# Kernel optimization log

Measured on AMD Instinct MI355X. Metric: run time of the kernel, lower is better.

The kernel has to match this reference:

```python
import jax, jax.numpy as jnp
import numpy as np

N_NODES = 100000
N_EDGES = 1600000
IN_CH, EDGE_DIM, HIDDEN, OUT_CH = 3, 3, 64, 1


def setup_inputs() -> dict:
    key = jax.random.key(0)
    ks = jax.random.split(key, 10)
    x = jax.random.normal(ks[0], (N_NODES, IN_CH), dtype=jnp.float32)
    edge_index = jax.random.randint(ks[1], (2, N_EDGES), 0, N_NODES, dtype=jnp.int64)
    edge_attr = jax.random.normal(ks[2], (N_EDGES, EDGE_DIM), dtype=jnp.float32)
    # Linear params (torch Linear: y = x @ W.T + b); we store W as (in, out)
    s1 = 1.0 / np.sqrt(IN_CH + EDGE_DIM)
    W1 = jax.random.uniform(ks[3], (IN_CH + EDGE_DIM, HIDDEN), jnp.float32, -s1, s1)
    b1 = jax.random.uniform(ks[4], (HIDDEN,), jnp.float32, -s1, s1)
    s2 = 1.0 / np.sqrt(HIDDEN + EDGE_DIM)
    W2 = jax.random.uniform(ks[5], (HIDDEN + EDGE_DIM, HIDDEN), jnp.float32, -s2, s2)
    b2 = jax.random.uniform(ks[6], (HIDDEN,), jnp.float32, -s2, s2)
    s3 = 1.0 / np.sqrt(HIDDEN)
    W3 = jax.random.uniform(ks[7], (HIDDEN, OUT_CH), jnp.float32, -s3, s3)
    b3 = jax.random.uniform(ks[8], (OUT_CH,), jnp.float32, -s3, s3)
    return {"x": x, "edge_index": edge_index, "edge_attr": edge_attr,
            "W1": W1, "b1": b1, "W2": W2, "b2": b2, "W3": W3, "b3": b3}


def _edge_conv(h, src, dst, edge_attr, W, b, n_nodes):
    # gather source node features, concat edge_attr, linear, scatter-add at dst
    msg = jnp.concatenate([h[src], edge_attr], axis=-1) @ W + b  # [E, out]
    return jax.ops.segment_sum(msg, dst, num_segments=n_nodes)   # [N, out]


def reference(x, edge_index, edge_attr, W1, b1, W2, b2, W3, b3):
    src, dst = edge_index[0], edge_index[1]  # PyG source_to_target: aggregate at edge_index[1]
    n = x.shape[0]
    h = jax.nn.relu(_edge_conv(x, src, dst, edge_attr, W1, b1, n))
    h = jax.nn.relu(_edge_conv(h, src, dst, edge_attr, W2, b2, n))
    return h @ W3 + b3  # (n_nodes, 1) anomaly logits
```

## Files before the change

kernel.cpp:

```cpp
#include <hip/hip_runtime.h>

#define N_NODES 100000
#define N_EDGES 1600000
#define NCHUNK 256
#define CHUNK_E (N_EDGES / NCHUNK)
#define BSHIFT 6
#define BMASK 63
#define NBUCK 1563
#define REC_CAP 1536


typedef unsigned int uint4_ev __attribute__((ext_vector_type(4)));
typedef short bf16x8 __attribute__((ext_vector_type(8)));
typedef float f32x4 __attribute__((ext_vector_type(4)));

__device__ __forceinline__ unsigned short f2bf(float f) {
    unsigned int u = __float_as_uint(f);
    unsigned int r = (u + 0x7fff + ((u >> 16) & 1)) >> 16;
    return (unsigned short)r;
}
__device__ __forceinline__ unsigned int pack2bf(float a, float b) {
    return (unsigned int)f2bf(a) | ((unsigned int)f2bf(b) << 16);
}
__device__ __forceinline__ float bflo(unsigned int v) { return __uint_as_float(v << 16); }
__device__ __forceinline__ float bfhi(unsigned int v) { return __uint_as_float(v & 0xffff0000u); }

__device__ __forceinline__ float4 nt_load4(const float4* p) {
    uint4_ev v = __builtin_nontemporal_load((const uint4_ev*)p);
    return make_float4(__uint_as_float(v.x), __uint_as_float(v.y),
                       __uint_as_float(v.z), __uint_as_float(v.w));
}

__device__ __forceinline__ int wave_incl_scan(int v, int lane) {
#pragma unroll
    for (int off = 1; off < 64; off <<= 1) {
        int t = __shfl_up(v, off, 64);
        if (lane >= off) v += t;
    }
    return v;
}

__global__ __launch_bounds__(1024) void k_hist(const int* __restrict__ ei,
                                               int* __restrict__ tbl,
                                               const float* __restrict__ W2,
                                               unsigned short* __restrict__ wpk) {
    if (blockIdx.x == NCHUNK) {
        int i = threadIdx.x;
        if (i < 512) {
            int lane = i & 63, hh = (i >> 6) & 1, nt = i >> 7;
            int col = nt * 16 + (lane & 15);
            int k0 = hh * 32 + (lane >> 4) * 8;
#pragma unroll
            for (int j = 0; j < 8; j++)
                wpk[i * 8 + j] = f2bf(W2[(k0 + j) * 64 + col]);
        }
        return;
    }
    __shared__ int h[NBUCK];
    for (int i = threadIdx.x; i < NBUCK; i += 1024) h[i] = 0;
    __syncthreads();
    const int base = blockIdx.x * CHUNK_E;
    for (int i = threadIdx.x; i < CHUNK_E; i += 1024)
        atomicAdd(&h[ei[N_EDGES + base + i] >> BSHIFT], 1);
    __syncthreads();
    for (int i = threadIdx.x; i < NBUCK; i += 1024)
        tbl[blockIdx.x * NBUCK + i] = h[i];
}

__global__ __launch_bounds__(256) void k_colscan(int* __restrict__ tbl,
                                                 int* __restrict__ bsum) {
    const int b = blockIdx.x, t = threadIdx.x;
    int v = tbl[t * NBUCK + b];
    int lane = t & 63, w = t >> 6;
    int inc = wave_incl_scan(v, lane);
    __shared__ int ws[4];
    if (lane == 63) ws[w] = inc;
    __syncthreads();
    int wo = 0;
    for (int k = 0; k < w; k++) wo += ws[k];
    tbl[t * NBUCK + b] = wo + inc - v;
    if (t == 255) bsum[b] = wo + inc;
}

__global__ __launch_bounds__(1024) void k_basescan(const int* __restrict__ bsum,
                                                   int* __restrict__ bbase) {
    int t = threadIdx.x, lane = t & 63, w = t >> 6;
    int i0 = 2 * t, i1 = 2 * t + 1;
    int v0 = (i0 < NBUCK) ? bsum[i0] : 0;
    int v1 = (i1 < NBUCK) ? bsum[i1] : 0;
    int s = v0 + v1;
    int inc = wave_incl_scan(s, lane);
    __shared__ int ws[16];
    if (lane == 63) ws[w] = inc;
    __syncthreads();
    int wo = 0;
    for (int k = 0; k < w; k++) wo += ws[k];
    int excl = wo + inc - s;
    if (i0 < NBUCK) bbase[i0] = excl;
    if (i1 < NBUCK) bbase[i1] = excl + v0;
    if (i0 == NBUCK - 1) bbase[NBUCK] = excl + v0;
}

__global__ __launch_bounds__(1024) void k_scatter(const int* __restrict__ ei,
                                                  const float* __restrict__ ea,
                                                  const int* __restrict__ tbl,
                                                  const int* __restrict__ bbase,
                                                  float4* __restrict__ stg) {
    __shared__ int cur[NBUCK];
    for (int i = threadIdx.x; i < NBUCK; i += 1024)
        cur[i] = tbl[blockIdx.x * NBUCK + i] + bbase[i];
    __syncthreads();
    const int base = blockIdx.x * CHUNK_E;
    for (int i = threadIdx.x; i < CHUNK_E; i += 1024) {
        int e = base + i;
        int src = ei[e];
        int dst = ei[N_EDGES + e];
        float a0 = ea[(size_t)e * 3 + 0];
        float a1 = ea[(size_t)e * 3 + 1];
        float a2 = ea[(size_t)e * 3 + 2];
        int p = atomicAdd(&cur[dst >> BSHIFT], 1);
        unsigned pk = (unsigned)src | ((unsigned)(dst & BMASK) << 17);
        stg[p] = make_float4(__uint_as_float(pk), a0, a1, a2);
    }
}

__global__ __launch_bounds__(256) void k_finalize(
    const float4* __restrict__ stg, const int* __restrict__ bbase,
    const float* __restrict__ x, int* __restrict__ csr,
    int* __restrict__ degp, int* __restrict__ rowend,
    float* __restrict__ U, float* __restrict__ T) {
    __shared__ float4 rec[REC_CAP];
    __shared__ int hist[64], lofs[64], cur[64];
    const int b = blockIdx.x, t = threadIdx.x;
    const int base = bbase[b], cnt = bbase[b + 1] - base;
    if (t < 64) hist[t] = 0;
    __syncthreads();
    const float* stgf = (const float*)stg;
    for (int i = t; i < cnt; i += 256) {
        unsigned pk = __float_as_uint(stgf[(size_t)(base + i) * 4]);
        atomicAdd(&hist[pk >> 17], 1);
    }
    __syncthreads();
    if (t < 64) {
        int v = hist[t];
        int inc = wave_incl_scan(v, t);
        lofs[t] = inc - v;
        cur[t] = inc - v;
    }
    __syncthreads();
    for (int i = t; i < cnt; i += 256) {
        float4 r = nt_load4(&stg[base + i]);
        unsigned pk = __float_as_uint(r.x);
        int p = atomicAdd(&cur[pk >> 17], 1);
        if (p < REC_CAP) rec[p] = r;
    }
    __syncthreads();
    const int l = t >> 2, sub = t & 3;
    const int n = b * 64 + l;
    const int d = hist[l], lo = lofs[l];
    float u0 = 0, u1 = 0, u2 = 0, t0 = 0, t1 = 0, t2 = 0;
    for (int j = sub; j < d; j += 4) {
        float4 r = rec[lo + j];
        unsigned pk = __float_as_uint(r.x);
        int src = pk & 0x1FFFF;
        csr[base + lo + j] = src;
        t0 += r.y; t1 += r.z; t2 += r.w;
        u0 += x[src * 3 + 0]; u1 += x[src * 3 + 1]; u2 += x[src * 3 + 2];
    }
#pragma unroll
    for (int off = 1; off <= 2; off <<= 1) {
        u0 += __shfl_xor(u0, off, 64); u1 += __shfl_xor(u1, off, 64);
        u2 += __shfl_xor(u2, off, 64); t0 += __shfl_xor(t0, off, 64);
        t1 += __shfl_xor(t1, off, 64); t2 += __shfl_xor(t2, off, 64);
    }
    if (sub == 0 && n < N_NODES) {
        degp[n] = d;
        rowend[n] = base + lo + d;
        U[n * 3 + 0] = u0; U[n * 3 + 1] = u1; U[n * 3 + 2] = u2;
        T[n * 3 + 0] = t0; T[n * 3 + 1] = t1; T[n * 3 + 2] = t2;
    }
}

__global__ __launch_bounds__(256) void k_h1z(
    const int* __restrict__ degp, const float* __restrict__ U,
    const float* __restrict__ T, const float* __restrict__ W1,
    const float* __restrict__ b1, const float* __restrict__ W2,
    const float* __restrict__ b2, const bf16x8* __restrict__ wpk,
    unsigned int* __restrict__ zu, unsigned int* __restrict__ eu) {
    const int lane = threadIdx.x & 63;
    const int base = (blockIdx.x * 4 + (threadIdx.x >> 6)) * 16;
    if (base >= N_NODES) return;
    const int col = lane & 15;
    const int q = lane >> 4;

    const int node = base + col;
    const float d = (float)degp[node];
    const float u0 = U[node * 3], u1 = U[node * 3 + 1], u2 = U[node * 3 + 2];
    const float t0 = T[node * 3], t1 = T[node * 3 + 1], t2 = T[node * 3 + 2];
    bf16x8 af[2];
#pragma unroll
    for (int h = 0; h < 2; h++) {
#pragma unroll
        for (int j = 0; j < 8; j++) {
            int c = h * 32 + q * 8 + j;
            float a = d * b1[c];
            a = fmaf(u0, W1[0 * 64 + c], a);
            a = fmaf(u1, W1[1 * 64 + c], a);
            a = fmaf(u2, W1[2 * 64 + c], a);
            a = fmaf(t0, W1[3 * 64 + c], a);
            a = fmaf(t1, W1[4 * 64 + c], a);
            a = fmaf(t2, W1[5 * 64 + c], a);
            af[h][j] = (short)f2bf(fmaxf(a, 0.f));
        }
    }

    f32x4 acc[4];
#pragma unroll
    for (int nt = 0; nt < 4; nt++) {
        bf16x8 b0 = wpk[(nt * 2 + 0) * 64 + lane];
        bf16x8 b1f = wpk[(nt * 2 + 1) * 64 + lane];
        f32x4 a = {0.f, 0.f, 0.f, 0.f};
        a = __builtin_amdgcn_mfma_f32_16x16x32_bf16(af[0], b0, a, 0, 0, 0);
        a = __builtin_amdgcn_mfma_f32_16x16x32_bf16(af[1], b1f, a, 0, 0, 0);
        acc[nt] = a;
    }
#pragma unroll
    for (int nt = 0; nt < 4; nt++) {
#pragma unroll
        for (int r = 0; r < 4; r++) {
            float v = acc[nt][r];
            float pv = __shfl_xor(v, 1, 64);
            if ((lane & 1) == 0) {
                int nr = base + q * 4 + r;
                zu[(size_t)nr * 32 + nt * 8 + (col >> 1)] = pack2bf(v, pv);
            }
        }
    }

    const float eb = b2[lane];
    const float w64 = W2[64 * 64 + lane];
    const float w65 = W2[65 * 64 + lane];
    const float w66 = W2[66 * 64 + lane];
#pragma unroll 4
    for (int mm = 0; mm < 16; mm++) {
        int nn = base + mm;
        float dd = (float)degp[nn];
        float s0 = T[nn * 3], s1 = T[nn * 3 + 1], s2 = T[nn * 3 + 2];
        float e = dd * eb;
        e = fmaf(s0, w64, e); e = fmaf(s1, w65, e); e = fmaf(s2, w66, e);
        float pe = __shfl_xor(e, 1, 64);
        if ((lane & 1) == 0)
            eu[(size_t)nn * 32 + (lane >> 1)] = pack2bf(e, pe);
    }
}

__global__ __launch_bounds__(256) void k_agg(
    const unsigned int* __restrict__ zu, const unsigned int* __restrict__ eu,
    const int* __restrict__ rowend, const int* __restrict__ degp,
    const int* __restrict__ csr, const float* __restrict__ W3,
    const float* __restrict__ b3, float* __restrict__ out) {
    const int lane = threadIdx.x & 63;
    const int li = lane & 15;
    const int q = li & 7;
    const int r = li >> 3;
    const int n = blockIdx.x * 16 + (threadIdx.x >> 4);

    float cw3[8];
#pragma unroll
    for (int m = 0; m < 8; m++) cw3[m] = W3[8 * q + m];
    const float b3v = b3[0];

    const int end = rowend[n], d = degp[n], start = end - d;
    float S[8];
#pragma unroll
    for (int m = 0; m < 8; m++) S[m] = 0.f;

    for (int c = start; c < end; c += 8) {
        int idx[4];
        float mk[4];
        uint4 v[4];
#pragma unroll
        for (int u = 0; u < 4; u++) {
            int i = c + 2 * u + r;
            bool ok = i < end;
            mk[u] = ok ? 1.f : 0.f;
            idx[u] = csr[ok ? i : start];
        }
#pragma unroll
        for (int u = 0; u < 4; u++)
            v[u] = *(const uint4*)&zu[(size_t)idx[u] * 32 + q * 4];
#pragma unroll
        for (int u = 0; u < 4; u++) {
            S[0] = fmaf(mk[u], bflo(v[u].x), S[0]); S[1] = fmaf(mk[u], bfhi(v[u].x), S[1]);
            S[2] = fmaf(mk[u], bflo(v[u].y), S[2]); S[3] = fmaf(mk[u], bfhi(v[u].y), S[3]);
            S[4] = fmaf(mk[u], bflo(v[u].z), S[4]); S[5] = fmaf(mk[u], bfhi(v[u].z), S[5]);
            S[6] = fmaf(mk[u], bflo(v[u].w), S[6]); S[7] = fmaf(mk[u], bfhi(v[u].w), S[7]);
        }
    }
#pragma unroll
    for (int m = 0; m < 8; m++) S[m] += __shfl_xor(S[m], 8, 64);

    const uint4 ev = *(const uint4*)&eu[(size_t)n * 32 + q * 4];
    float contrib;
    {
        float h0 = fmaxf(S[0] + bflo(ev.x), 0.f);
        float h1v = fmaxf(S[1] + bfhi(ev.x), 0.f);
        float h2v = fmaxf(S[2] + bflo(ev.y), 0.f);
        float h3 = fmaxf(S[3] + bfhi(ev.y), 0.f);
        float h4 = fmaxf(S[4] + bflo(ev.z), 0.f);
        float h5 = fmaxf(S[5] + bfhi(ev.z), 0.f);
        float h6 = fmaxf(S[6] + bflo(ev.w), 0.f);
        float h7 = fmaxf(S[7] + bfhi(ev.w), 0.f);
        contrib = h0 * cw3[0];
        contrib = fmaf(h1v, cw3[1], contrib);
        contrib = fmaf(h2v, cw3[2], contrib);
        contrib = fmaf(h3, cw3[3], contrib);
        contrib = fmaf(h4, cw3[4], contrib);
        contrib = fmaf(h5, cw3[5], contrib);
        contrib = fmaf(h6, cw3[6], contrib);
        contrib = fmaf(h7, cw3[7], contrib);
    }
    contrib += __shfl_xor(contrib, 1, 64);
    contrib += __shfl_xor(contrib, 2, 64);
    contrib += __shfl_xor(contrib, 4, 64);
    if (li == 0) out[n] = contrib + b3v;
}

extern "C" void kernel_launch(void* const* d_in, const int* in_sizes, int n_in,
                              void* d_out, int out_size, void* d_ws, size_t ws_size,
                              hipStream_t stream) {
    const float* x  = (const float*)d_in[0];
    const int*   ei = (const int*)d_in[1];
    const float* ea = (const float*)d_in[2];
    const float* W1 = (const float*)d_in[3];
    const float* b1 = (const float*)d_in[4];
    const float* W2 = (const float*)d_in[5];
    const float* b2 = (const float*)d_in[6];
    const float* W3 = (const float*)d_in[7];
    const float* b3 = (const float*)d_in[8];
    float* out = (float*)d_out;

    char* ws = (char*)d_ws;
    int*    tbl    = (int*)(ws + 0);
    int*    bsum   = (int*)(ws + 1600512);
    int*    bbase  = (int*)(ws + 1606912);
    int*    degp   = (int*)(ws + 1613312);
    int*    rowend = (int*)(ws + 2013440);
    float*  U      = (float*)(ws + 2413568);
    float*  T      = (float*)(ws + 3613696);
    int*    csr    = (int*)(ws + 4813824);
    float4* stg    = (float4*)(ws + 11213824);
    unsigned int* zu = (unsigned int*)(ws + 11213824);
    unsigned int* eu = (unsigned int*)(ws + 24013824);
    unsigned short* wpk = (unsigned short*)(ws + 36813824);

    k_hist<<<NCHUNK + 1, 1024, 0, stream>>>(ei, tbl, W2, wpk);
    k_colscan<<<NBUCK, 256, 0, stream>>>(tbl, bsum);
    k_basescan<<<1, 1024, 0, stream>>>(bsum, bbase);
    k_scatter<<<NCHUNK, 1024, 0, stream>>>(ei, ea, tbl, bbase, stg);
    k_finalize<<<NBUCK, 256, 0, stream>>>(stg, bbase, x, csr, degp, rowend, U, T);
    k_h1z<<<1563, 256, 0, stream>>>(degp, U, T, W1, b1, W2, b2,
                                    (const bf16x8*)wpk, zu, eu);
    k_agg<<<N_NODES / 16, 256, 0, stream>>>(zu, eu, rowend, degp, csr, W3, b3, out);
}
```

Measured before the change: 194.1 us.

## Fuse h1/z computation into finalize, double chunk count, unroll aggregation

```diff
diff --git a/kernel.cpp b/kernel.cpp
--- a/kernel.cpp
+++ b/kernel.cpp
@@ -2,7 +2,7 @@
 
 #define N_NODES 100000
 #define N_EDGES 1600000
-#define NCHUNK 256
+#define NCHUNK 512
 #define CHUNK_E (N_EDGES / NCHUNK)
 #define BSHIFT 6
 #define BMASK 63
@@ -67,19 +67,19 @@
         tbl[blockIdx.x * NBUCK + i] = h[i];
 }
 
-__global__ __launch_bounds__(256) void k_colscan(int* __restrict__ tbl,
+__global__ __launch_bounds__(512) void k_colscan(int* __restrict__ tbl,
                                                  int* __restrict__ bsum) {
     const int b = blockIdx.x, t = threadIdx.x;
     int v = tbl[t * NBUCK + b];
     int lane = t & 63, w = t >> 6;
     int inc = wave_incl_scan(v, lane);
-    __shared__ int ws[4];
+    __shared__ int ws[8];
     if (lane == 63) ws[w] = inc;
     __syncthreads();
     int wo = 0;
     for (int k = 0; k < w; k++) wo += ws[k];
     tbl[t * NBUCK + b] = wo + inc - v;
-    if (t == 255) bsum[b] = wo + inc;
+    if (t == 511) bsum[b] = wo + inc;
 }
 
 __global__ __launch_bounds__(1024) void k_basescan(const int* __restrict__ bsum,
@@ -126,11 +126,14 @@
 
 __global__ __launch_bounds__(256) void k_finalize(
     const float4* __restrict__ stg, const int* __restrict__ bbase,
-    const float* __restrict__ x, int* __restrict__ csr,
-    int* __restrict__ degp, int* __restrict__ rowend,
-    float* __restrict__ U, float* __restrict__ T) {
+    const float* __restrict__ x, const float* __restrict__ W1,
+    const float* __restrict__ b1, const float* __restrict__ W2,
+    const float* __restrict__ b2, const bf16x8* __restrict__ wpk,
+    int* __restrict__ csr, int* __restrict__ degp, int* __restrict__ rowend,
+    unsigned int* __restrict__ zu, unsigned int* __restrict__ eu) {
     __shared__ float4 rec[REC_CAP];
     __shared__ int hist[64], lofs[64], cur[64];
+    __shared__ float sU[64 * 3], sT[64 * 3];
     const int b = blockIdx.x, t = threadIdx.x;
     const int base = bbase[b], cnt = bbase[b + 1] - base;
     if (t < 64) hist[t] = 0;
@@ -155,48 +158,44 @@
         if (p < REC_CAP) rec[p] = r;
     }
     __syncthreads();
-    const int l = t >> 2, sub = t & 3;
-    const int n = b * 64 + l;
-    const int d = hist[l], lo = lofs[l];
-    float u0 = 0, u1 = 0, u2 = 0, t0 = 0, t1 = 0, t2 = 0;
-    for (int j = sub; j < d; j += 4) {
-        float4 r = rec[lo + j];
-        unsigned pk = __float_as_uint(r.x);
-        int src = pk & 0x1FFFF;
-        csr[base + lo + j] = src;
-        t0 += r.y; t1 += r.z; t2 += r.w;
-        u0 += x[src * 3 + 0]; u1 += x[src * 3 + 1]; u2 += x[src * 3 + 2];
-    }
-#pragma unroll
-    for (int off = 1; off <= 2; off <<= 1) {
-        u0 += __shfl_xor(u0, off, 64); u1 += __shfl_xor(u1, off, 64);
-        u2 += __shfl_xor(u2, off, 64); t0 += __shfl_xor(t0, off, 64);
-        t1 += __shfl_xor(t1, off, 64); t2 += __shfl_xor(t2, off, 64);
-    }
-    if (sub == 0 && n < N_NODES) {
-        degp[n] = d;
-        rowend[n] = base + lo + d;
-        U[n * 3 + 0] = u0; U[n * 3 + 1] = u1; U[n * 3 + 2] = u2;
-        T[n * 3 + 0] = t0; T[n * 3 + 1] = t1; T[n * 3 + 2] = t2;
-    }
-}
-
-__global__ __launch_bounds__(256) void k_h1z(
-    const int* __restrict__ degp, const float* __restrict__ U,
-    const float* __restrict__ T, const float* __restrict__ W1,
-    const float* __restrict__ b1, const float* __restrict__ W2,
-    const float* __restrict__ b2, const bf16x8* __restrict__ wpk,
-    unsigned int* __restrict__ zu, unsigned int* __restrict__ eu) {
-    const int lane = threadIdx.x & 63;
-    const int base = (blockIdx.x * 4 + (threadIdx.x >> 6)) * 16;
-    if (base >= N_NODES) return;
+    {
+        const int l = t >> 2, sub = t & 3;
+        const int n = b * 64 + l;
+        const int d = hist[l], lo = lofs[l];
+        float u0 = 0, u1 = 0, u2 = 0, t0 = 0, t1 = 0, t2 = 0;
+        for (int j = sub; j < d; j += 4) {
+            float4 r = rec[lo + j];
+            unsigned pk = __float_as_uint(r.x);
+            int src = pk & 0x1FFFF;
+            csr[base + lo + j] = src;
+            t0 += r.y; t1 += r.z; t2 += r.w;
+            u0 += x[src * 3 + 0]; u1 += x[src * 3 + 1]; u2 += x[src * 3 + 2];
+        }
+#pragma unroll
+        for (int off = 1; off <= 2; off <<= 1) {
+            u0 += __shfl_xor(u0, off, 64); u1 += __shfl_xor(u1, off, 64);
+            u2 += __shfl_xor(u2, off, 64); t0 += __shfl_xor(t0, off, 64);
+            t1 += __shfl_xor(t1, off, 64); t2 += __shfl_xor(t2, off, 64);
+        }
+        if (sub == 0) {
+            sU[l * 3 + 0] = u0; sU[l * 3 + 1] = u1; sU[l * 3 + 2] = u2;
+            sT[l * 3 + 0] = t0; sT[l * 3 + 1] = t1; sT[l * 3 + 2] = t2;
+            if (n < N_NODES) {
+                degp[n] = d;
+                rowend[n] = base + lo + d;
+            }
+        }
+    }
+    __syncthreads();
+    const int lane = t & 63, w = t >> 6;
+    const int tb = b * 64 + w * 16;
+    if (tb >= N_NODES) return;
     const int col = lane & 15;
     const int q = lane >> 4;
-
-    const int node = base + col;
-    const float d = (float)degp[node];
-    const float u0 = U[node * 3], u1 = U[node * 3 + 1], u2 = U[node * 3 + 2];
-    const float t0 = T[node * 3], t1 = T[node * 3 + 1], t2 = T[node * 3 + 2];
+    const int ln = w * 16 + col;
+    const float d = (float)hist[ln];
+    const float u0 = sU[ln * 3], u1 = sU[ln * 3 + 1], u2 = sU[ln * 3 + 2];
+    const float t0 = sT[ln * 3], t1 = sT[ln * 3 + 1], t2 = sT[ln * 3 + 2];
     bf16x8 af[2];
 #pragma unroll
     for (int h = 0; h < 2; h++) {
@@ -213,7 +212,6 @@
             af[h][j] = (short)f2bf(fmaxf(a, 0.f));
         }
     }
-
     f32x4 acc[4];
 #pragma unroll
     for (int nt = 0; nt < 4; nt++) {
@@ -231,26 +229,25 @@
             float v = acc[nt][r];
             float pv = __shfl_xor(v, 1, 64);
             if ((lane & 1) == 0) {
-                int nr = base + q * 4 + r;
+                int nr = tb + q * 4 + r;
                 zu[(size_t)nr * 32 + nt * 8 + (col >> 1)] = pack2bf(v, pv);
             }
         }
     }
-
     const float eb = b2[lane];
     const float w64 = W2[64 * 64 + lane];
     const float w65 = W2[65 * 64 + lane];
     const float w66 = W2[66 * 64 + lane];
 #pragma unroll 4
     for (int mm = 0; mm < 16; mm++) {
-        int nn = base + mm;
-        float dd = (float)degp[nn];
-        float s0 = T[nn * 3], s1 = T[nn * 3 + 1], s2 = T[nn * 3 + 2];
+        int lm = w * 16 + mm;
+        float dd = (float)hist[lm];
+        float s0 = sT[lm * 3], s1 = sT[lm * 3 + 1], s2 = sT[lm * 3 + 2];
         float e = dd * eb;
         e = fmaf(s0, w64, e); e = fmaf(s1, w65, e); e = fmaf(s2, w66, e);
         float pe = __shfl_xor(e, 1, 64);
         if ((lane & 1) == 0)
-            eu[(size_t)nn * 32 + (lane >> 1)] = pack2bf(e, pe);
+            eu[(size_t)(tb + mm) * 32 + (lane >> 1)] = pack2bf(e, pe);
     }
 }
 
@@ -275,22 +272,22 @@
 #pragma unroll
     for (int m = 0; m < 8; m++) S[m] = 0.f;
 
-    for (int c = start; c < end; c += 8) {
-        int idx[4];
-        float mk[4];
-        uint4 v[4];
-#pragma unroll
-        for (int u = 0; u < 4; u++) {
+    for (int c = start; c < end; c += 16) {
+        int idx[8];
+        float mk[8];
+        uint4 v[8];
+#pragma unroll
+        for (int u = 0; u < 8; u++) {
             int i = c + 2 * u + r;
             bool ok = i < end;
             mk[u] = ok ? 1.f : 0.f;
             idx[u] = csr[ok ? i : start];
         }
 #pragma unroll
-        for (int u = 0; u < 4; u++)
+        for (int u = 0; u < 8; u++)
             v[u] = *(const uint4*)&zu[(size_t)idx[u] * 32 + q * 4];
 #pragma unroll
-        for (int u = 0; u < 4; u++) {
+        for (int u = 0; u < 8; u++) {
             S[0] = fmaf(mk[u], bflo(v[u].x), S[0]); S[1] = fmaf(mk[u], bfhi(v[u].x), S[1]);
             S[2] = fmaf(mk[u], bflo(v[u].y), S[2]); S[3] = fmaf(mk[u], bfhi(v[u].y), S[3]);
             S[4] = fmaf(mk[u], bflo(v[u].z), S[4]); S[5] = fmaf(mk[u], bfhi(v[u].z), S[5]);
@@ -342,24 +339,21 @@
 
     char* ws = (char*)d_ws;
     int*    tbl    = (int*)(ws + 0);
-    int*    bsum   = (int*)(ws + 1600512);
-    int*    bbase  = (int*)(ws + 1606912);
-    int*    degp   = (int*)(ws + 1613312);
-    int*    rowend = (int*)(ws + 2013440);
-    float*  U      = (float*)(ws + 2413568);
-    float*  T      = (float*)(ws + 3613696);
-    int*    csr    = (int*)(ws + 4813824);
-    float4* stg    = (float4*)(ws + 11213824);
-    unsigned int* zu = (unsigned int*)(ws + 11213824);
-    unsigned int* eu = (unsigned int*)(ws + 24013824);
-    unsigned short* wpk = (unsigned short*)(ws + 36813824);
+    int*    bsum   = (int*)(ws + 3201024);
+    int*    bbase  = (int*)(ws + 3207424);
+    int*    degp   = (int*)(ws + 3213824);
+    int*    rowend = (int*)(ws + 3613952);
+    int*    csr    = (int*)(ws + 4014080);
+    float4* stg    = (float4*)(ws + 10414080);
+    unsigned int* zu = (unsigned int*)(ws + 36014080);
+    unsigned int* eu = (unsigned int*)(ws + 48814080);
+    unsigned short* wpk = (unsigned short*)(ws + 61614080);
 
     k_hist<<<NCHUNK + 1, 1024, 0, stream>>>(ei, tbl, W2, wpk);
-    k_colscan<<<NBUCK, 256, 0, stream>>>(tbl, bsum);
+    k_colscan<<<NBUCK, 512, 0, stream>>>(tbl, bsum);
     k_basescan<<<1, 1024, 0, stream>>>(bsum, bbase);
     k_scatter<<<NCHUNK, 1024, 0, stream>>>(ei, ea, tbl, bbase, stg);
-    k_finalize<<<NBUCK, 256, 0, stream>>>(stg, bbase, x, csr, degp, rowend, U, T);
-    k_h1z<<<1563, 256, 0, stream>>>(degp, U, T, W1, b1, W2, b2,
-                                    (const bf16x8*)wpk, zu, eu);
+    k_finalize<<<NBUCK, 256, 0, stream>>>(stg, bbase, x, W1, b1, W2, b2,
+                                          (const bf16x8*)wpk, csr, degp, rowend, zu, eu);
     k_agg<<<N_NODES / 16, 256, 0, stream>>>(zu, eu, rowend, degp, csr, W3, b3, out);
 }
```

After: 202.4 us. +4.3%, slower.
